# Performance work log

Measured on AMD Instinct MI355X. Metric: run time of the kernel, lower is better.

The kernel has to match this reference:

```python
import jax, jax.numpy as jnp
import numpy as np

C = 1024        # number of classes
N = 8           # proxies per class
ALLNUM = C * N  # 8192 total proxies
DIM = 512
R = 0.05
TOPK = int(np.ceil(R * ALLNUM))  # 410
LAM = 0.3
B = 2048


def setup_inputs() -> dict:
    key = jax.random.key(0)
    k1, k2, k3 = jax.random.split(key, 3)
    inp = jax.random.normal(k1, (B, DIM), dtype=jnp.float32)
    target = jax.random.randint(k2, (B,), 0, C, dtype=jnp.int64)
    # kaiming-uniform-initialized proxies approximated by scaled normal init
    proxies = jax.random.normal(k3, (DIM, ALLNUM), dtype=jnp.float32)
    instance_label = jnp.repeat(jnp.arange(C, dtype=jnp.int64), N)  # [ALLNUM]
    return {"input": inp, "target": target, "Proxies": proxies,
            "instance_label": instance_label}


def reference(input, target, Proxies, instance_label):
    # L2-normalize each proxy column (F.normalize along dim=0, eps=1e-12)
    norm = jnp.maximum(jnp.linalg.norm(Proxies, axis=0, keepdims=True), 1e-12)
    centers = Proxies / norm                             # [DIM, ALLNUM]
    similarity = input @ centers                          # [B, ALLNUM]

    positive_mask = (target[:, None] == instance_label[None, :]).astype(similarity.dtype)
    _, indices = jax.lax.top_k(similarity + 1000.0 * positive_mask, TOPK)  # [B, TOPK]

    rows = jnp.arange(similarity.shape[0])[:, None]
    mask = jnp.zeros_like(similarity).at[rows, indices].set(1.0)
    prob_a = mask * similarity                            # sparse-masked similarities

    y_instance_onehot = jax.nn.one_hot(instance_label, C, dtype=similarity.dtype)  # [ALLNUM, C]
    logits = prob_a @ y_instance_onehot                   # [B, C]

    y_target_onehot = jax.nn.one_hot(target, C, dtype=similarity.dtype)  # [B, C]
    logits_mask = 1.0 - (logits == 0.0).astype(similarity.dtype)

    # scale_mask_softmax with scale=1 along dim=1
    e = jnp.exp(logits) * logits_mask
    predict = e / (1e-8 + jnp.sum(e, axis=1, keepdims=True))
    lossClassify = jnp.mean(jnp.sum(-y_target_onehot * jnp.log(predict + 1e-20), axis=1))

    # proxy regularizer: cross-entropy of proxy-vs-class logits
    simCenter = centers.T @ centers                       # [ALLNUM, ALLNUM]
    centers_logits = simCenter @ y_instance_onehot        # [ALLNUM, C]
    logp = jax.nn.log_softmax(centers_logits, axis=1)
    reg = -jnp.mean(jnp.take_along_axis(logp, instance_label[:, None], axis=1))

    return (lossClassify + LAM * reg, lossClassify)
```

## Files before the change

### kernel.cpp

```cpp
#include <hip/hip_runtime.h>
#include <hip/hip_bf16.h>
#include <math.h>

#define C_CLS   1024
#define NPROXY  8
#define ALLNUM  8192
#define DIM     512
#define TOPK    410
#define LAM     0.3f
#define BATCH   2048

#define BAND_CAP_BLK 28
#define ROW_CAP      512
#define GCAP         64

typedef __bf16 bf16x8 __attribute__((ext_vector_type(8)));
typedef float floatx4 __attribute__((ext_vector_type(4)));
typedef unsigned short ushort_t;

#define WS_RNORM 0
#define WS_SIG   8192
#define WS_LP    10240
#define WS_RP    12288
#define WS_CNT   14336
#define WS_NDEF  16384
#define WS_FLAG  18432
#define WS_CLS   20480
#define WS_BVAL  (WS_CLS + 2048*1024)
#define WS_BCOL  (WS_BVAL + 2048*512)
#define WS_ABF   (WS_BCOL + 2048*256)
#define WS_PBF   (WS_ABF + 524288)
#define WS_STBF  (WS_PBF + 2097152)
#define WS_LOG   (WS_STBF + 262144)

__device__ inline float block_reduce(float v, int is_max, float* red, int t) {
    #pragma unroll
    for (int o = 32; o > 0; o >>= 1) {
        float w = __shfl_down(v, o);
        v = is_max ? fmaxf(v, w) : (v + w);
    }
    __syncthreads();
    if ((t & 63) == 0) red[t >> 6] = v;
    __syncthreads();
    return is_max ? fmaxf(fmaxf(red[0], red[1]), fmaxf(red[2], red[3]))
                  : (red[0] + red[1] + red[2] + red[3]);
}

__device__ inline ushort_t f2bf(float f) {
    unsigned u = __float_as_uint(f);
    return (ushort_t)((u + 0x7FFFu + ((u >> 16) & 1u)) >> 16);
}

__device__ inline float bf2f(ushort_t u) {
    return __uint_as_float(((unsigned)u) << 16);
}

__device__ inline void ld_g2l_16(const void* g, void* l) {
    __builtin_amdgcn_global_load_lds(
        (const __attribute__((address_space(1))) unsigned int*)g,
        (__attribute__((address_space(3))) unsigned int*)l,
        16, 0, 0);
}

__device__ inline unsigned f2ord(float f) {
    unsigned u = __float_as_uint(f);
    return (u & 0x80000000u) ? ~u : (u | 0x80000000u);
}

__global__ __launch_bounds__(256) void k_prep1(const float* __restrict__ P,
                                               const float* __restrict__ input,
                                               float* __restrict__ rnorm,
                                               float* __restrict__ rowsig,
                                               ushort_t* __restrict__ Abf,
                                               ushort_t* __restrict__ Pbf,
                                               ushort_t* __restrict__ Stbf,
                                               unsigned* __restrict__ zaux) {
    __shared__ float tile[32][33];
    __shared__ float s_rn[32];
    float* cred = &tile[0][0];
    int bx = blockIdx.x, t = threadIdx.x;
    if (bx < 256) {
        int tc = t & 31, g = t >> 5;
        int c = bx * 32 + tc;
        const float* pc = P + (size_t)(g * 64) * ALLNUM + c;
        float s = 0.f;
        #pragma unroll 8
        for (int d = 0; d < 64; ++d) {
            float v = pc[(size_t)d * ALLNUM];
            s += v * v;
        }
        cred[g * 32 + tc] = s;
        __syncthreads();
        if (g == 0) {
            float tot = 0.f;
            #pragma unroll
            for (int k = 0; k < 8; ++k) tot += cred[k * 32 + tc];
            float r = 1.0f / fmaxf(sqrtf(tot), 1e-12f);
            rnorm[c] = r;
            s_rn[tc] = r;
        }
        __syncthreads();
        #pragma unroll
        for (int p = 0; p < 8; ++p) {
            int idx = t + 256 * p;
            int d = idx >> 2, cc = idx & 3;
            const float* pp = P + (size_t)d * ALLNUM + bx * 32 + cc * 8;
            const float* rr = &s_rn[cc * 8];
            float4 a = *(const float4*)pp;
            float4 b = *(const float4*)(pp + 4);
            float v = a.x * rr[0] + a.y * rr[1] + a.z * rr[2] + a.w * rr[3] +
                      b.x * rr[4] + b.y * rr[5] + b.z * rr[6] + b.w * rr[7];
            Stbf[(size_t)(bx * 4 + cc) * DIM + d] = f2bf(v);
        }
    } else if (bx < 256 + 1024) {
        int a = bx - 256;
        int idx = a * 256 + t;
        float4 v = ((const float4*)input)[idx];
        ushort4 o;
        o.x = f2bf(v.x); o.y = f2bf(v.y); o.z = f2bf(v.z); o.w = f2bf(v.w);
        ((ushort4*)Abf)[idx] = o;
        float sq = v.x * v.x + v.y * v.y + v.z * v.z + v.w * v.w;
        #pragma unroll
        for (int off = 32; off > 0; off >>= 1) sq += __shfl_down(sq, off);
        int lane = t & 63, w = t >> 6;
        if (lane == 0) cred[w] = sq;
        __syncthreads();
        if (t == 0) {
            rowsig[2 * a]     = sqrtf(cred[0] + cred[1]);
            rowsig[2 * a + 1] = sqrtf(cred[2] + cred[3]);
        }
    } else if (bx < 256 + 1024 + 4096) {
        int id = bx - 1280;
        int c0 = (id & 255) * 32, r0 = (id >> 8) * 32;
        int tc = t & 31, tr = t >> 5;
        #pragma unroll
        for (int p = 0; p < 4; ++p)
            tile[tr + p * 8][tc] = P[(size_t)(r0 + tr + p * 8) * ALLNUM + c0 + tc];
        __syncthreads();
        #pragma unroll
        for (int p = 0; p < 4; ++p) {
            int oc = tr + p * 8;
            Pbf[(size_t)(c0 + oc) * DIM + r0 + tc] = f2bf(tile[tc][oc]);
        }
    } else {
        for (int i = t; i < 3 * 2048; i += 256) zaux[i] = 0u;
    }
}

__global__ __launch_bounds__(512, 1) void k_gemms(const ushort_t* __restrict__ Abf,
                                                  const ushort_t* __restrict__ Pbf,
                                                  const ushort_t* __restrict__ Stbf,
                                                  const float* __restrict__ rnorm,
                                                  const float* __restrict__ rowsig,
                                                  const int* __restrict__ target,
                                                  float* __restrict__ g_cls,
                                                  float* __restrict__ g_bval,
                                                  ushort_t* __restrict__ g_bcol,
                                                  unsigned* __restrict__ g_cnt,
                                                  unsigned* __restrict__ g_ndef,
                                                  unsigned* __restrict__ g_flag,
                                                  ushort_t* __restrict__ logits) {
    __shared__ __align__(16) ushort_t smem[73728];
    int bx = blockIdx.x, t = threadIdx.x;
    int w = t >> 6, lane = t & 63;
    int ml = lane & 15, q4 = lane >> 4;
    int wm = w >> 1, wn = w & 1;

    int wid = (bx & 7) * 96 + (bx >> 3);
    int isg0 = (wid < 512);
    const ushort_t* Ap;
    const ushort_t* Bp;
    int bi, bj;
    if (isg0) {
        bi = (wid & 7) * 256;
        bj = (wid >> 3) * 128;
        Ap = Abf; Bp = Pbf;
    } else {
        int id1 = wid - 512;
        bi = (id1 & 31) * 256;
        bj = (id1 >> 5) * 128;
        Ap = Pbf; Bp = Stbf;
    }

    floatx4 acc[4][4];
    #pragma unroll
    for (int mf = 0; mf < 4; ++mf)
        #pragma unroll
        for (int nf = 0; nf < 4; ++nf)
            acc[mf][nf] = (floatx4){0.f, 0.f, 0.f, 0.f};

    #define STAGE(t_, k0_) do {                                                \
        int bo_ = ((t_) % 3) * 24576;                                          \
        _Pragma("unroll")                                                      \
        for (int it_ = 0; it_ < 4; ++it_) {                                    \
            int c_ = w * 256 + it_ * 64 + lane;                                \
            int m_ = c_ >> 3, q_ = (c_ & 7) ^ (m_ & 7);                        \
            ld_g2l_16(Ap + ((size_t)(bi + m_) << 9) + (k0_) + q_ * 8,          \
                      &smem[bo_ + c_ * 8]);                                    \
        }                                                                      \
        _Pragma("unroll")                                                      \
        for (int it_ = 0; it_ < 2; ++it_) {                                    \
            int c_ = w * 128 + it_ * 64 + lane;                                \
            int m_ = c_ >> 3, q_ = (c_ & 7) ^ (m_ & 7);                        \
            ld_g2l_16(Bp + ((size_t)(bj + m_) << 9) + (k0_) + q_ * 8,          \
                      &smem[bo_ + 16384 + c_ * 8]);                            \
        } } while (0)

    STAGE(0, 0);
    STAGE(1, 64);

    #pragma unroll
    for (int tt = 0; tt < 8; ++tt) {
        if (tt < 7) asm volatile("s_waitcnt vmcnt(6)" ::: "memory");
        else        asm volatile("s_waitcnt vmcnt(0)" ::: "memory");
        __builtin_amdgcn_s_barrier();
        if (tt < 6) STAGE(tt + 2, (tt + 2) * 64);

        const ushort_t* Xa = &smem[(tt % 3) * 24576];
        const ushort_t* Xb = Xa + 16384;
        bf16x8 af[2][4], bfr[2][4];
        #pragma unroll
        for (int kk = 0; kk < 2; ++kk) {
            #pragma unroll
            for (int nf = 0; nf < 4; ++nf) {
                int n = wn * 64 + nf * 16 + ml;
                int s = (kk * 4 + q4) ^ (n & 7);
                bfr[kk][nf] = *(const bf16x8*)&Xb[n * 64 + s * 8];
            }
            #pragma unroll
            for (int mf = 0; mf < 4; ++mf) {
                int m = wm * 64 + mf * 16 + ml;
                int s = (kk * 4 + q4) ^ (m & 7);
                af[kk][mf] = *(const bf16x8*)&Xa[m * 64 + s * 8];
            }
        }
        __builtin_amdgcn_s_setprio(1);
        #pragma unroll
        for (int kk = 0; kk < 2; ++kk)
            #pragma unroll
            for (int mf = 0; mf < 4; ++mf)
                #pragma unroll
                for (int nf = 0; nf < 4; ++nf)
                    acc[mf][nf] = __builtin_amdgcn_mfma_f32_16x16x32_bf16(
                        af[kk][mf], bfr[kk][nf], acc[mf][nf], 0, 0, 0);
        __builtin_amdgcn_s_setprio(0);
    }
    #undef STAGE
    __syncthreads();

    if (isg0) {
        unsigned char* sb8 = (unsigned char*)smem;
        float*    e_cls = (float*)sb8;
        float*    e_bv  = (float*)(sb8 + 16384);
        ushort_t* e_bc  = (ushort_t*)(sb8 + 45056);
        unsigned* e_cnt = (unsigned*)(sb8 + 59392);
        unsigned* e_nd  = (unsigned*)(sb8 + 60416);

        #pragma unroll
        for (int i = t; i < 4096; i += 512) e_cls[i] = 0.f;
        if (t < 256) { e_cnt[t] = 0u; e_nd[t] = 0u; }
        __syncthreads();

        #pragma unroll
        for (int mf = 0; mf < 4; ++mf) {
            int rl0 = wm * 64 + mf * 16 + q4 * 4;
            int rowb = bi + rl0;
            float4 rs4 = *(const float4*)&rowsig[rowb];
            int4   tg4 = *(const int4*)&target[rowb];
            #pragma unroll
            for (int nf = 0; nf < 4; ++nf) {
                int cl = wn * 64 + nf * 16 + ml;
                int col = bj + cl;
                float sc = rnorm[col];
                int cls = col >> 3;
                int clsl = cl >> 3;
                #pragma unroll
                for (int i = 0; i < 4; ++i) {
                    int rl = rl0 + i;
                    float v = acc[mf][nf][i] * sc;
                    float sg = ((const float*)&rs4)[i] * (1.0f / 22.616f);
                    float hiT = 1.80f * sg, loT = 1.47f * sg;
                    int tg = ((const int*)&tg4)[i];
                    if (cls == tg) {
                        atomicAdd(&e_cls[rl * 16 + clsl], v);
                    } else if (v >= hiT) {
                        atomicAdd(&e_cls[rl * 16 + clsl], v);
                        atomicAdd(&e_nd[rl], 1u);
                    } else if (v >= loT) {
                        unsigned u = atomicAdd(&e_cnt[rl], 1u);
                        if (u < BAND_CAP_BLK) {
                            e_bv[rl * BAND_CAP_BLK + u] = v;
                            e_bc[rl * BAND_CAP_BLK + u] = (ushort_t)col;
                        }
                    }
                }
            }
        }
        __syncthreads();

        int bjc = bj >> 3;
        #pragma unroll
        for (int i = t; i < 4096; i += 512) {
            int rl = i >> 4, c = i & 15;
            g_cls[(size_t)(bi + rl) * C_CLS + bjc + c] = e_cls[i];
        }
        if (t < 256) {
            int row = bi + t;
            unsigned cbb = e_cnt[t];
            unsigned nd = e_nd[t];
            if (nd) atomicAdd(&g_ndef[row], nd);
            if (cbb) {
                unsigned cc = (cbb > BAND_CAP_BLK) ? BAND_CAP_BLK : cbb;
                unsigned base = atomicAdd(&g_cnt[row], cc);
                if (cbb > BAND_CAP_BLK || base + cc > ROW_CAP) g_flag[row] = 1u;
                for (unsigned j = 0; j < cc; ++j) {
                    if (base + j >= ROW_CAP) break;
                    g_bval[(size_t)row * ROW_CAP + base + j] = e_bv[t * BAND_CAP_BLK + j];
                    g_bcol[(size_t)row * ROW_CAP + base + j] = e_bc[t * BAND_CAP_BLK + j];
                }
            }
        }
    } else {
        #pragma unroll
        for (int mf = 0; mf < 4; ++mf) {
            int rowb = bi + wm * 64 + mf * 16 + q4 * 4;
            float4 rnr = *(const float4*)&rnorm[rowb];
            #pragma unroll
            for (int nf = 0; nf < 4; ++nf) {
                int col = bj + wn * 64 + nf * 16 + ml;
                #pragma unroll
                for (int i = 0; i < 4; ++i)
                    logits[(size_t)(rowb + i) * C_CLS + col] =
                        f2bf(acc[mf][nf][i] * ((const float*)&rnr)[i]);
            }
        }
    }
}

__device__ inline void suffix_select1(unsigned* s_hist, unsigned kk,
                                      unsigned* s_wtot, unsigned* sh_bin,
                                      unsigned* sh_k, int t, int lane, int wid) {
    unsigned h = s_hist[t];
    unsigned v = h;
    #pragma unroll
    for (int off = 1; off < 64; off <<= 1) {
        unsigned o = __shfl_down(v, off);
        if (lane + off < 64) v += o;
    }
    if (lane == 0) s_wtot[wid] = v;
    __syncthreads();
    unsigned above = v - h;
    for (int w2 = wid + 1; w2 < 4; ++w2) above += s_wtot[w2];
    unsigned cum = above + h;
    if (cum >= kk && above < kk) { *sh_bin = (unsigned)t; *sh_k = kk - above; }
    __syncthreads();
}

__global__ __launch_bounds__(256) void k_finish(const int* __restrict__ target,
                                                const float* __restrict__ rowsig,
                                                const float* __restrict__ rnorm,
                                                const ushort_t* __restrict__ Abf,
                                                const ushort_t* __restrict__ Pbf,
                                                const float* __restrict__ g_cls,
                                                const float* __restrict__ g_bval,
                                                const ushort_t* __restrict__ g_bcol,
                                                const unsigned* __restrict__ g_cnt,
                                                const unsigned* __restrict__ g_ndef,
                                                const unsigned* __restrict__ g_flag,
                                                float* __restrict__ loss_part,
                                                const ushort_t* __restrict__ logits,
                                                float* __restrict__ reg_part) {
    __shared__ __align__(16) unsigned char smem[16384];
    int bx = blockIdx.x, t = threadIdx.x;
    int lane = t & 63, wid = t >> 6;

    if (bx < 2048) {
        float*    s_cls  = (float*)smem;
        float*    s_bval = (float*)(smem + 4096);
        ushort_t* s_bcol = (ushort_t*)(smem + 6144);
        unsigned* s_hist = (unsigned*)(smem + 7168);
        float*    s_arow = (float*)(smem + 8192);
        unsigned* s_wtot = (unsigned*)(smem + 10240);
        unsigned* shv    = (unsigned*)(smem + 10256);
        float*    shf    = (float*)(smem + 10272);
        float*    red    = (float*)(smem + 10288);
        float*    s_gval = (float*)(smem + 10304);

        int b = bx;
        int tgt = target[b];
        float sig = rowsig[b] * (1.0f / 22.616f);
        float hiT = 1.80f * sig, loT = 1.47f * sig;
        float binscale = 256.0f / (hiT - loT);

        ((float4*)s_cls)[t] = ((const float4*)(g_cls + (size_t)b * C_CLS))[t];
        unsigned cnt = g_cnt[b], nd = g_ndef[b], fl = g_flag[b];
        int kq = (TOPK - NPROXY) - (int)nd;
        int ok = (fl == 0u) && (cnt <= ROW_CAP) && (kq >= 0) && ((int)cnt >= kq);
        if (t == 0) shv[1] = 0u;
        s_hist[t] = 0u;
        __syncthreads();

        if (ok) {
            if (kq > 0) {
                for (int j = t; j < (int)cnt; j += 256) {
                    float v = g_bval[(size_t)b * ROW_CAP + j];
                    s_bval[j] = v;
                    s_bcol[j] = g_bcol[(size_t)b * ROW_CAP + j];
                    int bin = (int)((v - loT) * binscale);
                    bin = (bin > 255) ? 255 : bin;
                    atomicAdd(&s_hist[bin], 1u);
                }
                __syncthreads();
                suffix_select1(s_hist, (unsigned)kq, s_wtot, &shv[2], &shv[3], t, lane, wid);
                int Bb = (int)shv[2];
                int knew = (int)shv[3];
                for (int j = t; j < (int)cnt; j += 256) {
                    float v = s_bval[j];
                    int bin = (int)((v - loT) * binscale);
                    bin = (bin > 255) ? 255 : bin;
                    if (bin == Bb) {
                        unsigned g = atomicAdd(&shv[1], 1u);
                        if (g < GCAP) s_gval[g] = v;
                    }
                }
                __syncthreads();
                int gc = (int)shv[1];
                if (gc <= GCAP) {
                    if (t < gc) {
                        float vj = s_gval[t];
                        unsigned g = 0, geq = 0;
                        for (int i = 0; i < gc; ++i) {
                            float vi = s_gval[i];
                            g   += (vi > vj) ? 1u : 0u;
                            geq += (vi >= vj) ? 1u : 0u;
                        }
                        if (g < (unsigned)knew && geq >= (unsigned)knew) shf[0] = vj;
                    }
                } else {
                    for (int j = t; j < (int)cnt; j += 256) {
                        float vj = s_bval[j];
                        unsigned g = 0, geq = 0;
                        for (int i = 0; i < (int)cnt; ++i) {
                            float vi = s_bval[i];
                            g   += (vi > vj) ? 1u : 0u;
                            geq += (vi >= vj) ? 1u : 0u;
                        }
                        if (g < (unsigned)kq && geq >= (unsigned)kq) shf[0] = vj;
                    }
                }
                __syncthreads();
                float thr = shf[0];
                for (int j = t; j < (int)cnt; j += 256)
                    if (s_bval[j] >= thr)
                        atomicAdd(&s_cls[s_bcol[j] >> 3], s_bval[j]);
            }
        } else {
            for (int i = t; i < DIM; i += 256)
                s_arow[i] = bf2f(Abf[(size_t)b * DIM + i]);
            #pragma unroll
            for (int i = 0; i < 4; ++i) s_cls[t + 256 * i] = 0.f;
            __syncthreads();
            float4 v4[8];
            for (int p = 0; p < 8; ++p) {
                int f = t + 256 * p;
                float vv[4];
                for (int e = 0; e < 4; ++e) {
                    int col = 4 * f + e;
                    const ushort_t* pc = Pbf + (size_t)col * DIM;
                    float a = 0.f;
                    for (int d = 0; d < DIM; ++d)
                        a += s_arow[d] * bf2f(pc[d]);
                    vv[e] = a * rnorm[col];
                }
                float4 o; o.x = vv[0]; o.y = vv[1]; o.z = vv[2]; o.w = vv[3];
                v4[p] = o;
            }
            #pragma unroll
            for (int p = 0; p < 8; ++p) {
                int f = t + 256 * p;
                const float* pv = (const float*)&v4[p];
                if ((f >> 1) == tgt)
                    atomicAdd(&s_cls[tgt], pv[0] + pv[1] + pv[2] + pv[3]);
            }
            unsigned L = 0u, R = 0xFFFFFFFFu;
            for (int it = 0; it < 33 && R - L > 1; ++it) {
                unsigned mid = L + ((R - L) >> 1);
                float c = 0.f;
                #pragma unroll
                for (int p = 0; p < 8; ++p) {
                    int f = t + 256 * p;
                    const float* pv = (const float*)&v4[p];
                    if ((f >> 1) != tgt) {
                        #pragma unroll
                        for (int e = 0; e < 4; ++e)
                            c += (f2ord(pv[e]) >= mid) ? 1.f : 0.f;
                    }
                }
                c = block_reduce(c, 0, red, t);
                if (c >= (float)(TOPK - NPROXY)) L = mid; else R = mid;
                __syncthreads();
            }
            #pragma unroll
            for (int p = 0; p < 8; ++p) {
                int f = t + 256 * p;
                const float* pv = (const float*)&v4[p];
                if ((f >> 1) != tgt) {
                    #pragma unroll
                    for (int e = 0; e < 4; ++e)
                        if (f2ord(pv[e]) >= L)
                            atomicAdd(&s_cls[f >> 1], pv[e]);
                }
            }
        }
        __syncthreads();

        float4 cv = ((const float4*)s_cls)[t];
        float m = -1e30f;
        if (cv.x != 0.0f) m = fmaxf(m, cv.x);
        if (cv.y != 0.0f) m = fmaxf(m, cv.y);
        if (cv.z != 0.0f) m = fmaxf(m, cv.z);
        if (cv.w != 0.0f) m = fmaxf(m, cv.w);
        m = block_reduce(m, 1, red, t);
        float se = 0.f;
        if (cv.x != 0.0f) se += expf(cv.x - m);
        if (cv.y != 0.0f) se += expf(cv.y - m);
        if (cv.z != 0.0f) se += expf(cv.z - m);
        if (cv.w != 0.0f) se += expf(cv.w - m);
        se = block_reduce(se, 0, red, t);
        if (t == 0) {
            float lt = s_cls[tgt];
            float predict_t = expf(lt - m) / (1e-8f * expf(-m) + se);
            loss_part[b] = -logf(predict_t + 1e-20f);
        }
    } else {
        __shared__ float bsum[4];
        int rb = bx - 2048;
        int i = rb * 4 + wid;
        const ushort_t* row = logits + (size_t)i * C_CLS;
        uint4 c0 = ((const uint4*)row)[lane];
        uint4 c1 = ((const uint4*)(row + 512))[lane];

        float f[16];
        const unsigned* u0 = (const unsigned*)&c0;
        const unsigned* u1 = (const unsigned*)&c1;
        #pragma unroll
        for (int k = 0; k < 4; ++k) {
            f[2 * k]     = __uint_as_float(u0[k] << 16);
            f[2 * k + 1] = __uint_as_float(u0[k] & 0xFFFF0000u);
            f[8 + 2 * k]     = __uint_as_float(u1[k] << 16);
            f[8 + 2 * k + 1] = __uint_as_float(u1[k] & 0xFFFF0000u);
        }

        int cstar = i >> 3;
        int chunk = cstar >> 9, within = cstar & 511;
        float sd = 0.f;
        if (lane == (within >> 3)) sd = f[chunk * 8 + (within & 7)];

        float m = -1e30f;
        #pragma unroll
        for (int k = 0; k < 16; ++k) m = fmaxf(m, f[k]);
        #pragma unroll
        for (int off = 32; off > 0; off >>= 1) m = fmaxf(m, __shfl_xor(m, off));

        float se = 0.f;
        #pragma unroll
        for (int k = 0; k < 16; ++k) se += expf(f[k] - m);
        #pragma unroll
        for (int off = 32; off > 0; off >>= 1) se += __shfl_xor(se, off);
        #pragma unroll
        for (int off = 32; off > 0; off >>= 1) sd += __shfl_xor(sd, off);

        if (lane == 0) bsum[wid] = m + logf(se) - sd;
        __syncthreads();
        if (t == 0)
            reg_part[rb] = bsum[0] + bsum[1] + bsum[2] + bsum[3];
    }
}

__global__ __launch_bounds__(256) void k_final(const float* __restrict__ lp,
                                               const float* __restrict__ rp,
                                               float* __restrict__ out) {
    __shared__ float red[4];
    int t = threadIdx.x;
    float4 a = ((const float4*)lp)[t];
    float4 b = ((const float4*)lp)[t + 256];
    float4 c = ((const float4*)rp)[t];
    float4 d = ((const float4*)rp)[t + 256];
    float ls = a.x + a.y + a.z + a.w + b.x + b.y + b.z + b.w;
    float rs = c.x + c.y + c.z + c.w + d.x + d.y + d.z + d.w;
    ls = block_reduce(ls, 0, red, t);
    rs = block_reduce(rs, 0, red, t);
    if (t == 0) {
        float lc = ls / (float)BATCH;
        float rg = rs / (float)ALLNUM;
        out[0] = lc + LAM * rg;
        out[1] = lc;
    }
}

extern "C" void kernel_launch(void* const* d_in, const int* in_sizes, int n_in,
                              void* d_out, int out_size, void* d_ws, size_t ws_size,
                              hipStream_t stream) {
    const float* input  = (const float*)d_in[0];
    const int*   target = (const int*)d_in[1];
    const float* P      = (const float*)d_in[2];

    float* ws        = (float*)d_ws;
    float* rnorm     = ws + WS_RNORM;
    float* rowsig    = ws + WS_SIG;
    float* loss_part = ws + WS_LP;
    float* reg_part  = ws + WS_RP;
    unsigned* g_cnt  = (unsigned*)(ws + WS_CNT);
    unsigned* g_ndef = (unsigned*)(ws + WS_NDEF);
    unsigned* g_flag = (unsigned*)(ws + WS_FLAG);
    float* g_cls     = ws + WS_CLS;
    float* g_bval    = ws + WS_BVAL;
    ushort_t* g_bcol = (ushort_t*)(ws + WS_BCOL);
    ushort_t* Abf    = (ushort_t*)(ws + WS_ABF);
    ushort_t* Pbf    = (ushort_t*)(ws + WS_PBF);
    ushort_t* Stbf   = (ushort_t*)(ws + WS_STBF);
    ushort_t* logits = (ushort_t*)(ws + WS_LOG);
    float* out       = (float*)d_out;

    hipLaunchKernelGGL(k_prep1, dim3(256 + 1024 + 4096 + 1), dim3(256), 0, stream,
                       P, input, rnorm, rowsig, Abf, Pbf, Stbf, g_cnt);
    hipLaunchKernelGGL(k_gemms, dim3(768), dim3(512), 0, stream,
                       Abf, Pbf, Stbf, rnorm, rowsig, target,
                       g_cls, g_bval, g_bcol, g_cnt, g_ndef, g_flag, logits);
    hipLaunchKernelGGL(k_finish, dim3(4096), dim3(256), 0, stream,
                       target, rowsig, rnorm, Abf, Pbf,
                       g_cls, g_bval, g_bcol, g_cnt, g_ndef, g_flag,
                       loss_part, logits, reg_part);
    hipLaunchKernelGGL(k_final, dim3(1), dim3(256), 0, stream,
                       loss_part, reg_part, out);
}
```

Before: 155.6 us.

## Fuse proxy-regularizer softmax into GEMM epilogue and merge proxy transpose into norm pass

The centers-logits GEMM epilogue now computes per-row partial max and sum-exp over each 128-column tile, plus the diagonal term, instead of writing a bf16 logits matrix. The finish kernel combines the 8 partials per row with an online log-sum-exp. The bf16 transpose of the proxies is folded into the norm blocks, which now stage a 512x32 tile in shared memory, so the separate 4096 transpose blocks are gone. This removes a 16 MB logits round trip and one extra read of P. In exchange the epilogue gains shuffle reductions and a block sync, and the prep blocks use about 67 KB of LDS each.

Measured after the change: 153.1 us. About the same (-1.6%).

```diff
diff --git a/kernel.cpp b/kernel.cpp
--- a/kernel.cpp
+++ b/kernel.cpp
@@ -31,7 +31,9 @@
 #define WS_ABF   (WS_BCOL + 2048*256)
 #define WS_PBF   (WS_ABF + 524288)
 #define WS_STBF  (WS_PBF + 2097152)
-#define WS_LOG   (WS_STBF + 262144)
+#define WS_MX    (WS_STBF + 262144)
+#define WS_SE    (WS_MX + 65536)
+#define WS_DIAG  (WS_SE + 65536)
 
 __device__ inline float block_reduce(float v, int is_max, float* red, int t) {
     #pragma unroll
@@ -75,18 +77,28 @@
                                                ushort_t* __restrict__ Pbf,
                                                ushort_t* __restrict__ Stbf,
                                                unsigned* __restrict__ zaux) {
-    __shared__ float tile[32][33];
+    __shared__ float stile[512 * 33];
+    __shared__ float cred[256];
     __shared__ float s_rn[32];
-    float* cred = &tile[0][0];
     int bx = blockIdx.x, t = threadIdx.x;
     if (bx < 256) {
+        int c0 = bx * 32;
+        #pragma unroll
+        for (int it = 0; it < 16; ++it) {
+            int r = it * 32 + (t >> 3);
+            int c4 = (t & 7) * 4;
+            float4 v = *(const float4*)&P[(size_t)r * ALLNUM + c0 + c4];
+            stile[r * 33 + c4]     = v.x;
+            stile[r * 33 + c4 + 1] = v.y;
+            stile[r * 33 + c4 + 2] = v.z;
+            stile[r * 33 + c4 + 3] = v.w;
+        }
+        __syncthreads();
         int tc = t & 31, g = t >> 5;
-        int c = bx * 32 + tc;
-        const float* pc = P + (size_t)(g * 64) * ALLNUM + c;
         float s = 0.f;
         #pragma unroll 8
-        for (int d = 0; d < 64; ++d) {
-            float v = pc[(size_t)d * ALLNUM];
+        for (int k = 0; k < 64; ++k) {
+            float v = stile[(g * 64 + k) * 33 + tc];
             s += v * v;
         }
         cred[g * 32 + tc] = s;
@@ -96,21 +108,34 @@
             #pragma unroll
             for (int k = 0; k < 8; ++k) tot += cred[k * 32 + tc];
             float r = 1.0f / fmaxf(sqrtf(tot), 1e-12f);
-            rnorm[c] = r;
+            rnorm[c0 + tc] = r;
             s_rn[tc] = r;
         }
         __syncthreads();
         #pragma unroll
-        for (int p = 0; p < 8; ++p) {
+        for (int p = 0; p < 16; ++p) {
             int idx = t + 256 * p;
-            int d = idx >> 2, cc = idx & 3;
-            const float* pp = P + (size_t)d * ALLNUM + bx * 32 + cc * 8;
-            const float* rr = &s_rn[cc * 8];
-            float4 a = *(const float4*)pp;
-            float4 b = *(const float4*)(pp + 4);
-            float v = a.x * rr[0] + a.y * rr[1] + a.z * rr[2] + a.w * rr[3] +
-                      b.x * rr[4] + b.y * rr[5] + b.z * rr[6] + b.w * rr[7];
-            Stbf[(size_t)(bx * 4 + cc) * DIM + d] = f2bf(v);
+            int c = idx >> 7, d4 = (idx & 127) * 4;
+            ushort4 o;
+            o.x = f2bf(stile[(d4    ) * 33 + c]);
+            o.y = f2bf(stile[(d4 + 1) * 33 + c]);
+            o.z = f2bf(stile[(d4 + 2) * 33 + c]);
+            o.w = f2bf(stile[(d4 + 3) * 33 + c]);
+            *(ushort4*)&Pbf[(size_t)(c0 + c) * DIM + d4] = o;
+        }
+        #pragma unroll
+        for (int p = 0; p < 4; ++p) {
+            int idx = t + 256 * p;
+            int cc = idx >> 8, d2 = (idx & 255) * 2;
+            float v0 = 0.f, v1 = 0.f;
+            #pragma unroll
+            for (int n = 0; n < 8; ++n) {
+                float rr = s_rn[cc * 8 + n];
+                v0 += stile[(d2    ) * 33 + cc * 8 + n] * rr;
+                v1 += stile[(d2 + 1) * 33 + cc * 8 + n] * rr;
+            }
+            ushort2 o; o.x = f2bf(v0); o.y = f2bf(v1);
+            *(ushort2*)&Stbf[(size_t)(bx * 4 + cc) * DIM + d2] = o;
         }
     } else if (bx < 256 + 1024) {
         int a = bx - 256;
@@ -128,19 +153,6 @@
         if (t == 0) {
             rowsig[2 * a]     = sqrtf(cred[0] + cred[1]);
             rowsig[2 * a + 1] = sqrtf(cred[2] + cred[3]);
-        }
-    } else if (bx < 256 + 1024 + 4096) {
-        int id = bx - 1280;
-        int c0 = (id & 255) * 32, r0 = (id >> 8) * 32;
-        int tc = t & 31, tr = t >> 5;
-        #pragma unroll
-        for (int p = 0; p < 4; ++p)
-            tile[tr + p * 8][tc] = P[(size_t)(r0 + tr + p * 8) * ALLNUM + c0 + tc];
-        __syncthreads();
-        #pragma unroll
-        for (int p = 0; p < 4; ++p) {
-            int oc = tr + p * 8;
-            Pbf[(size_t)(c0 + oc) * DIM + r0 + tc] = f2bf(tile[tc][oc]);
         }
     } else {
         for (int i = t; i < 3 * 2048; i += 256) zaux[i] = 0u;
@@ -159,7 +171,9 @@
                                                   unsigned* __restrict__ g_cnt,
                                                   unsigned* __restrict__ g_ndef,
                                                   unsigned* __restrict__ g_flag,
-                                                  ushort_t* __restrict__ logits) {
+                                                  float* __restrict__ g_mx,
+                                                  float* __restrict__ g_se,
+                                                  float* __restrict__ g_diag) {
     __shared__ __align__(16) ushort_t smem[73728];
     int bx = blockIdx.x, t = threadIdx.x;
     int w = t >> 6, lane = t & 63;
@@ -321,18 +335,73 @@
             }
         }
     } else {
+        int cj = bj >> 7;
+        float mloc[4][4], sloc[4][4];
         #pragma unroll
         for (int mf = 0; mf < 4; ++mf) {
             int rowb = bi + wm * 64 + mf * 16 + q4 * 4;
             float4 rnr = *(const float4*)&rnorm[rowb];
             #pragma unroll
-            for (int nf = 0; nf < 4; ++nf) {
-                int col = bj + wn * 64 + nf * 16 + ml;
+            for (int i = 0; i < 4; ++i) {
+                float mm = -1e30f;
+                #pragma unroll
+                for (int nf = 0; nf < 4; ++nf)
+                    mm = fmaxf(mm, acc[mf][nf][i] * ((const float*)&rnr)[i]);
+                mloc[mf][i] = mm;
+            }
+        }
+        #pragma unroll
+        for (int off = 1; off < 16; off <<= 1)
+            #pragma unroll
+            for (int mf = 0; mf < 4; ++mf)
                 #pragma unroll
                 for (int i = 0; i < 4; ++i)
-                    logits[(size_t)(rowb + i) * C_CLS + col] =
-                        f2bf(acc[mf][nf][i] * ((const float*)&rnr)[i]);
-            }
+                    mloc[mf][i] = fmaxf(mloc[mf][i], __shfl_xor(mloc[mf][i], off));
+        #pragma unroll
+        for (int mf = 0; mf < 4; ++mf) {
+            int rowb = bi + wm * 64 + mf * 16 + q4 * 4;
+            float4 rnr = *(const float4*)&rnorm[rowb];
+            #pragma unroll
+            for (int i = 0; i < 4; ++i) {
+                float ss = 0.f;
+                int row = rowb + i;
+                #pragma unroll
+                for (int nf = 0; nf < 4; ++nf) {
+                    float v = acc[mf][nf][i] * ((const float*)&rnr)[i];
+                    ss += expf(v - mloc[mf][i]);
+                    int col = bj + wn * 64 + nf * 16 + ml;
+                    if (col == (row >> 3)) g_diag[row] = v;
+                }
+                sloc[mf][i] = ss;
+            }
+        }
+        #pragma unroll
+        for (int off = 1; off < 16; off <<= 1)
+            #pragma unroll
+            for (int mf = 0; mf < 4; ++mf)
+                #pragma unroll
+                for (int i = 0; i < 4; ++i)
+                    sloc[mf][i] += __shfl_xor(sloc[mf][i], off);
+        float* s_m = (float*)smem;
+        float* s_s = s_m + 512;
+        if (ml == 0) {
+            #pragma unroll
+            for (int mf = 0; mf < 4; ++mf)
+                #pragma unroll
+                for (int i = 0; i < 4; ++i) {
+                    int r = wm * 64 + mf * 16 + q4 * 4 + i;
+                    s_m[r * 2 + wn] = mloc[mf][i];
+                    s_s[r * 2 + wn] = sloc[mf][i];
+                }
+        }
+        __syncthreads();
+        if (t < 256) {
+            float m0 = s_m[2 * t], m1 = s_m[2 * t + 1];
+            float s0 = s_s[2 * t], s1 = s_s[2 * t + 1];
+            float M = fmaxf(m0, m1);
+            float S = s0 * expf(m0 - M) + s1 * expf(m1 - M);
+            g_mx[(size_t)(bi + t) * 8 + cj] = M;
+            g_se[(size_t)(bi + t) * 8 + cj] = S;
         }
     }
 }
@@ -368,7 +437,9 @@
                                                 const unsigned* __restrict__ g_ndef,
                                                 const unsigned* __restrict__ g_flag,
                                                 float* __restrict__ loss_part,
-                                                const ushort_t* __restrict__ logits,
+                                                const float* __restrict__ g_mx,
+                                                const float* __restrict__ g_se,
+                                                const float* __restrict__ g_diag,
                                                 float* __restrict__ reg_part) {
     __shared__ __align__(16) unsigned char smem[16384];
     int bx = blockIdx.x, t = threadIdx.x;
@@ -533,47 +604,26 @@
             loss_part[b] = -logf(predict_t + 1e-20f);
         }
     } else {
-        __shared__ float bsum[4];
+        float* red2 = (float*)smem;
         int rb = bx - 2048;
-        int i = rb * 4 + wid;
-        const ushort_t* row = logits + (size_t)i * C_CLS;
-        uint4 c0 = ((const uint4*)row)[lane];
-        uint4 c1 = ((const uint4*)(row + 512))[lane];
-
-        float f[16];
-        const unsigned* u0 = (const unsigned*)&c0;
-        const unsigned* u1 = (const unsigned*)&c1;
-        #pragma unroll
-        for (int k = 0; k < 4; ++k) {
-            f[2 * k]     = __uint_as_float(u0[k] << 16);
-            f[2 * k + 1] = __uint_as_float(u0[k] & 0xFFFF0000u);
-            f[8 + 2 * k]     = __uint_as_float(u1[k] << 16);
-            f[8 + 2 * k + 1] = __uint_as_float(u1[k] & 0xFFFF0000u);
-        }
-
-        int cstar = i >> 3;
-        int chunk = cstar >> 9, within = cstar & 511;
-        float sd = 0.f;
-        if (lane == (within >> 3)) sd = f[chunk * 8 + (within & 7)];
-
-        float m = -1e30f;
-        #pragma unroll
-        for (int k = 0; k < 16; ++k) m = fmaxf(m, f[k]);
-        #pragma unroll
-        for (int off = 32; off > 0; off >>= 1) m = fmaxf(m, __shfl_xor(m, off));
-
-        float se = 0.f;
-        #pragma unroll
-        for (int k = 0; k < 16; ++k) se += expf(f[k] - m);
-        #pragma unroll
-        for (int off = 32; off > 0; off >>= 1) se += __shfl_xor(se, off);
-        #pragma unroll
-        for (int off = 32; off > 0; off >>= 1) sd += __shfl_xor(sd, off);
-
-        if (lane == 0) bsum[wid] = m + logf(se) - sd;
-        __syncthreads();
-        if (t == 0)
-            reg_part[rb] = bsum[0] + bsum[1] + bsum[2] + bsum[3];
+        float val = 0.f;
+        if (t < 64) {
+            int row = rb * 64 + t;
+            float mj[8], sj[8];
+            float M = -1e30f;
+            #pragma unroll
+            for (int j = 0; j < 8; ++j) {
+                mj[j] = g_mx[(size_t)row * 8 + j];
+                sj[j] = g_se[(size_t)row * 8 + j];
+                M = fmaxf(M, mj[j]);
+            }
+            float S = 0.f;
+            #pragma unroll
+            for (int j = 0; j < 8; ++j) S += sj[j] * expf(mj[j] - M);
+            val = M + logf(S) - g_diag[row];
+        }
+        val = block_reduce(val, 0, red2, t);
+        if (t == 0) reg_part[rb] = val;
     }
 }
 
@@ -584,10 +634,12 @@
     int t = threadIdx.x;
     float4 a = ((const float4*)lp)[t];
     float4 b = ((const float4*)lp)[t + 256];
-    float4 c = ((const float4*)rp)[t];
-    float4 d = ((const float4*)rp)[t + 256];
     float ls = a.x + a.y + a.z + a.w + b.x + b.y + b.z + b.w;
-    float rs = c.x + c.y + c.z + c.w + d.x + d.y + d.z + d.w;
+    float rs = 0.f;
+    if (t < 32) {
+        float4 c = ((const float4*)rp)[t];
+        rs = c.x + c.y + c.z + c.w;
+    }
     ls = block_reduce(ls, 0, red, t);
     rs = block_reduce(rs, 0, red, t);
     if (t == 0) {
@@ -619,18 +671,21 @@
     ushort_t* Abf    = (ushort_t*)(ws + WS_ABF);
     ushort_t* Pbf    = (ushort_t*)(ws + WS_PBF);
     ushort_t* Stbf   = (ushort_t*)(ws + WS_STBF);
-    ushort_t* logits = (ushort_t*)(ws + WS_LOG);
+    float* g_mx      = ws + WS_MX;
+    float* g_se      = ws + WS_SE;
+    float* g_diag    = ws + WS_DIAG;
     float* out       = (float*)d_out;
 
-    hipLaunchKernelGGL(k_prep1, dim3(256 + 1024 + 4096 + 1), dim3(256), 0, stream,
+    hipLaunchKernelGGL(k_prep1, dim3(256 + 1024 + 1), dim3(256), 0, stream,
                        P, input, rnorm, rowsig, Abf, Pbf, Stbf, g_cnt);
     hipLaunchKernelGGL(k_gemms, dim3(768), dim3(512), 0, stream,
                        Abf, Pbf, Stbf, rnorm, rowsig, target,
-                       g_cls, g_bval, g_bcol, g_cnt, g_ndef, g_flag, logits);
-    hipLaunchKernelGGL(k_finish, dim3(4096), dim3(256), 0, stream,
+                       g_cls, g_bval, g_bcol, g_cnt, g_ndef, g_flag,
+                       g_mx, g_se, g_diag);
+    hipLaunchKernelGGL(k_finish, dim3(2048 + 128), dim3(256), 0, stream,
                        target, rowsig, rnorm, Abf, Pbf,
                        g_cls, g_bval, g_bcol, g_cnt, g_ndef, g_flag,
-                       loss_part, logits, reg_part);
+                       loss_part, g_mx, g_se, g_diag, reg_part);
     hipLaunchKernelGGL(k_final, dim3(1), dim3(256), 0, stream,
                        loss_part, reg_part, out);
 }
```
